# Kernel tuning notes

Measured on AMD Instinct MI355X. Metric: run time of the kernel, lower is better.

Reference implementation:

```python
import jax, jax.numpy as jnp
import numpy as np

B, L, H, E, R = 2, 512, 768, 512, 32768
H2 = H // 2


def setup_inputs() -> dict:
    key = jax.random.key(0)
    ks = jax.random.split(key, 16)
    s = 0.02
    inp = {
        "hidden_states": jax.random.normal(ks[0], (B, L, H), dtype=jnp.float32),
        "ent_start": jax.random.randint(ks[1], (B, E), 0, L, dtype=jnp.int32),
        "ent_label": jax.random.randint(ks[2], (B, E), 0, 3, dtype=jnp.int32),
        "rel_head": jax.random.randint(ks[3], (B, R), 0, E, dtype=jnp.int32),
        "rel_tail": jax.random.randint(ks[4], (B, R), 0, E, dtype=jnp.int32),
        "rel_label": jax.random.randint(ks[5], (B, R), 0, 2, dtype=jnp.int32),
        "entity_emb": jax.random.normal(ks[6], (3, H), dtype=jnp.float32) * s,
        "head_W1": jax.random.normal(ks[7], (2 * H, H), dtype=jnp.float32) * s,
        "head_b1": jnp.zeros((H,), dtype=jnp.float32),
        "head_W2": jax.random.normal(ks[8], (H, H2), dtype=jnp.float32) * s,
        "head_b2": jnp.zeros((H2,), dtype=jnp.float32),
        "tail_W1": jax.random.normal(ks[9], (2 * H, H), dtype=jnp.float32) * s,
        "tail_b1": jnp.zeros((H,), dtype=jnp.float32),
        "tail_W2": jax.random.normal(ks[10], (H, H2), dtype=jnp.float32) * s,
        "tail_b2": jnp.zeros((H2,), dtype=jnp.float32),
        "bil_W": jax.random.normal(ks[11], (2, H2, H2), dtype=jnp.float32) * s,
        "lin_W": jax.random.normal(ks[12], (2 * H2, 2), dtype=jnp.float32) * s,
        "lin_b": jnp.zeros((2,), dtype=jnp.float32),
    }
    return inp


def _mlp(x, W1, b1, W2, b2):
    # Linear -> ReLU -> (dropout=identity) -> Linear -> ReLU -> (dropout=identity)
    h = jax.nn.relu(jnp.einsum("brd,dh->brh", x, W1) + b1)
    return jax.nn.relu(jnp.einsum("brh,hk->brk", h, W2) + b2)


def reference(hidden_states, ent_start, ent_label, rel_head, rel_tail, rel_label,
              entity_emb, head_W1, head_b1, head_W2, head_b2,
              tail_W1, tail_b1, tail_W2, tail_b2, bil_W, lin_W, lin_b):
    # Gather entity start token index and label for each relation endpoint
    h_idx = jnp.take_along_axis(ent_start, rel_head, axis=1)  # [B,R]
    t_idx = jnp.take_along_axis(ent_start, rel_tail, axis=1)
    h_lab = jnp.take_along_axis(ent_label, rel_head, axis=1)
    t_lab = jnp.take_along_axis(ent_label, rel_tail, axis=1)

    # Gather hidden states at entity start positions: [B,R,H]
    h_tok = jnp.take_along_axis(hidden_states, h_idx[..., None], axis=1)
    t_tok = jnp.take_along_axis(hidden_states, t_idx[..., None], axis=1)

    head_repr = jnp.concatenate([h_tok, entity_emb[h_lab]], axis=-1)  # [B,R,2H]
    tail_repr = jnp.concatenate([t_tok, entity_emb[t_lab]], axis=-1)

    heads = _mlp(head_repr, head_W1, head_b1, head_W2, head_b2)  # [B,R,H2]
    tails = _mlp(tail_repr, tail_W1, tail_b1, tail_W2, tail_b2)

    # BiaffineAttention: bilinear(x1,x2) + linear(cat(x1,x2))
    bil = jnp.einsum("brd,ode,bre->bro", heads, bil_W, tails)  # [B,R,2]
    lin = jnp.einsum("brc,co->bro", jnp.concatenate([heads, tails], axis=-1), lin_W) + lin_b
    logits = bil + lin  # [B,R,2]

    # Per-doc mean cross-entropy, summed over docs (matches loss accumulation)
    logp = jax.nn.log_softmax(logits, axis=-1)
    ce = -jnp.take_along_axis(logp, rel_label[..., None], axis=-1)[..., 0]  # [B,R]
    loss = ce.mean(axis=-1).sum()

    return loss, logits.reshape(B * R, 2)
```

## Files before the change

### kernel.cpp

```cpp
#include <hip/hip_runtime.h>
#include <math.h>

#define BB 2
#define LL 512
#define HH 768
#define EE 512
#define RR 32768
#define H2 384
#define MM 1024

typedef __attribute__((ext_vector_type(8))) short     bf16x8;
typedef __attribute__((ext_vector_type(4))) float     f32x4;
typedef __attribute__((ext_vector_type(8))) unsigned short u16x8;

#define BUFE (64 * 72)

__device__ __forceinline__ unsigned short f2bf(float f) {
    unsigned int u = __float_as_uint(f);
    u = (u + 0x7FFFu + ((u >> 16) & 1u)) >> 16;
    return (unsigned short)u;
}

__device__ __forceinline__ void wtrans(const float* __restrict__ src,
                                       unsigned short* __restrict__ dst,
                                       int K, int N, int tile, unsigned short* T)
{
    const int t = threadIdx.x;
    const int tn = N >> 5;
    const int n0 = (tile % tn) * 32;
    const int k0 = (tile / tn) * 32;
    const int r  = t >> 3;
    const int c4 = (t & 7) * 4;
    const float4 g = *(const float4*)(src + (size_t)(k0 + r) * N + n0 + c4);
    T[(c4 + 0) * 40 + r] = f2bf(g.x);
    T[(c4 + 1) * 40 + r] = f2bf(g.y);
    T[(c4 + 2) * 40 + r] = f2bf(g.z);
    T[(c4 + 3) * 40 + r] = f2bf(g.w);
    __syncthreads();
    const int n  = t >> 3;
    const int k4 = (t & 7) * 4;
    *(ushort4*)(dst + (size_t)(n0 + n) * K + k0 + k4) = *(ushort4*)&T[n * 40 + k4];
}

__global__ __launch_bounds__(256) void prep(
    const float* __restrict__ hW1, const float* __restrict__ tW1,
    unsigned short* __restrict__ W1ht, unsigned short* __restrict__ W1tt,
    const float* __restrict__ hidden, const int* __restrict__ ent_start,
    const float* __restrict__ emb,
    const float* __restrict__ hb1, const float* __restrict__ tb1,
    unsigned short* __restrict__ Hbf, float* __restrict__ embc,
    float* __restrict__ hlin, float* __restrict__ tlin, float* __restrict__ out)
{
    __shared__ unsigned short T[32 * 40];
    __shared__ float red[4][192];
    const int bid = blockIdx.x;
    const int t = threadIdx.x;

    if (bid == 2200) {
        const float4 z = {0.f, 0.f, 0.f, 0.f};
        ((float4*)hlin)[t] = z; ((float4*)hlin)[256 + t] = z;
        ((float4*)tlin)[t] = z; ((float4*)tlin)[256 + t] = z;
        if (t == 0) out[0] = 0.f;
        return;
    }

    if (bid >= 2176) {
        const int eb = bid - 2176;
        const int tc = t & 63;
        const int kg = t >> 6;
        const int n = eb * 64 + tc;
        const float* W = (n < 768) ? hW1 : tW1;
        const int cc = (n < 768) ? n : n - 768;
        float a0 = 0.f, a1 = 0.f, a2 = 0.f;
        const int kbeg = kg * 192;
        #pragma unroll 8
        for (int k = kbeg; k < kbeg + 192; ++k) {
            const float w = W[(size_t)(768 + k) * 768 + cc];
            a0 += emb[k] * w;
            a1 += emb[768 + k] * w;
            a2 += emb[1536 + k] * w;
        }
        red[kg][0 * 64 + tc] = a0;
        red[kg][1 * 64 + tc] = a1;
        red[kg][2 * 64 + tc] = a2;
        __syncthreads();
        if (kg == 0) {
            const float b = (n < 768) ? hb1[n] : tb1[n - 768];
            #pragma unroll
            for (int l = 0; l < 3; ++l) {
                embc[l * 1536 + n] = b + red[0][l * 64 + tc] + red[1][l * 64 + tc]
                                       + red[2][l * 64 + tc] + red[3][l * 64 + tc];
            }
        }
        return;
    }

    if (bid >= 1152) {
        const int m = bid - 1152;
        if (t >= 96) return;
        const int b = m >> 9;
        const int idx = ent_start[m];
        const float4* s = (const float4*)(hidden + (size_t)(b * LL + idx) * HH);
        const float4 v0 = s[2 * t];
        const float4 v1 = s[2 * t + 1];
        u16x8 o;
        o[0] = f2bf(v0.x); o[1] = f2bf(v0.y); o[2] = f2bf(v0.z); o[3] = f2bf(v0.w);
        o[4] = f2bf(v1.x); o[5] = f2bf(v1.y); o[6] = f2bf(v1.z); o[7] = f2bf(v1.w);
        *(u16x8*)(Hbf + (size_t)m * 768 + 8 * t) = o;
        return;
    }

    if (bid < 576) wtrans(hW1, W1ht, 768, 768, bid, T);
    else           wtrans(tW1, W1tt, 768, 768, bid - 576, T);
}

template<bool RELU, bool BIAS, bool EB, bool WF32, bool WBF16, bool O2, bool LIN>
__device__ __forceinline__ void gemm_body(
    int tile, int nx,
    const unsigned short* __restrict__ A, int lda, int aoff1,
    const unsigned short* __restrict__ Bt0, const unsigned short* __restrict__ Bt1,
    int ldb, int bt_mrow, int Nh,
    const float* __restrict__ bias0, const float* __restrict__ bias1,
    const float* __restrict__ embc, const int* __restrict__ labels,
    const float* __restrict__ linW, float* __restrict__ hlin, float* __restrict__ tlin,
    int K, float* __restrict__ Cf, unsigned short* __restrict__ Cb, int ldc,
    unsigned short* As, unsigned short* Bs)
{
    const int tid = threadIdx.x;
    const int n0 = (tile % nx) * 64;
    const int m0 = (tile / nx) * 64;
    const int hf = (n0 >= Nh) ? 1 : 0;
    const unsigned short* Bt = hf ? Bt1 : Bt0;
    const int nc0 = n0 - (hf ? Nh : 0);
    const int aoff = hf ? aoff1 : 0;

    const int sr = tid >> 2;
    const int sk = (tid & 3) * 16;

    const unsigned short* Ap = A + (size_t)(m0 + sr) * lda + aoff + sk;
    const unsigned short* Bp = Bt + (size_t)((m0 >> 9) * bt_mrow + nc0 + sr) * ldb + sk;

    const int lane = tid & 63;
    const int wave = tid >> 6;
    const int wm = (wave & 1) * 32;
    const int wn = (wave >> 1) * 32;
    const int l15 = lane & 15;
    const int quad = lane >> 4;
    const int swo = sr * 72 + sk;
    const int aro = quad * 8;

    f32x4 acc00 = {}, acc01 = {}, acc10 = {}, acc11 = {};

    u16x8 pa0, pa1, pb0, pb1;
    u16x8 qa0, qa1, qb0, qb1;

#define GLOADP(ko) { pa0 = *(const u16x8*)(Ap + (ko)); pa1 = *(const u16x8*)(Ap + (ko) + 8); \
                     pb0 = *(const u16x8*)(Bp + (ko)); pb1 = *(const u16x8*)(Bp + (ko) + 8); }
#define GLOADQ(ko) { qa0 = *(const u16x8*)(Ap + (ko)); qa1 = *(const u16x8*)(Ap + (ko) + 8); \
                     qb0 = *(const u16x8*)(Bp + (ko)); qb1 = *(const u16x8*)(Bp + (ko) + 8); }
#define SWRITEP(bi) { unsigned short* Aw = As + (bi) * BUFE; unsigned short* Bw = Bs + (bi) * BUFE; \
                      *(u16x8*)&Aw[swo] = pa0; *(u16x8*)&Aw[swo + 8] = pa1; \
                      *(u16x8*)&Bw[swo] = pb0; *(u16x8*)&Bw[swo + 8] = pb1; }
#define SWRITEQ(bi) { unsigned short* Aw = As + (bi) * BUFE; unsigned short* Bw = Bs + (bi) * BUFE; \
                      *(u16x8*)&Aw[swo] = qa0; *(u16x8*)&Aw[swo + 8] = qa1; \
                      *(u16x8*)&Bw[swo] = qb0; *(u16x8*)&Bw[swo + 8] = qb1; }
#define BAR() { asm volatile("s_waitcnt lgkmcnt(0)" ::: "memory"); \
                __builtin_amdgcn_s_barrier(); \
                __builtin_amdgcn_sched_barrier(0); }
#define MFMA8(bi) { const unsigned short* Ac = As + (bi) * BUFE; \
                    const unsigned short* Bc = Bs + (bi) * BUFE; \
        const bf16x8 fa0 = *(const bf16x8*)&Ac[(wm + l15) * 72 + aro]; \
        const bf16x8 fa1 = *(const bf16x8*)&Ac[(wm + 16 + l15) * 72 + aro]; \
        const bf16x8 fb0 = *(const bf16x8*)&Bc[(wn + l15) * 72 + aro]; \
        const bf16x8 fb1 = *(const bf16x8*)&Bc[(wn + 16 + l15) * 72 + aro]; \
        const bf16x8 ga0 = *(const bf16x8*)&Ac[(wm + l15) * 72 + aro + 32]; \
        const bf16x8 ga1 = *(const bf16x8*)&Ac[(wm + 16 + l15) * 72 + aro + 32]; \
        const bf16x8 gb0 = *(const bf16x8*)&Bc[(wn + l15) * 72 + aro + 32]; \
        const bf16x8 gb1 = *(const bf16x8*)&Bc[(wn + 16 + l15) * 72 + aro + 32]; \
        acc00 = __builtin_amdgcn_mfma_f32_16x16x32_bf16(fa0, fb0, acc00, 0, 0, 0); \
        acc01 = __builtin_amdgcn_mfma_f32_16x16x32_bf16(fa0, fb1, acc01, 0, 0, 0); \
        acc10 = __builtin_amdgcn_mfma_f32_16x16x32_bf16(fa1, fb0, acc10, 0, 0, 0); \
        acc11 = __builtin_amdgcn_mfma_f32_16x16x32_bf16(fa1, fb1, acc11, 0, 0, 0); \
        acc00 = __builtin_amdgcn_mfma_f32_16x16x32_bf16(ga0, gb0, acc00, 0, 0, 0); \
        acc01 = __builtin_amdgcn_mfma_f32_16x16x32_bf16(ga0, gb1, acc01, 0, 0, 0); \
        acc10 = __builtin_amdgcn_mfma_f32_16x16x32_bf16(ga1, gb0, acc10, 0, 0, 0); \
        acc11 = __builtin_amdgcn_mfma_f32_16x16x32_bf16(ga1, gb1, acc11, 0, 0, 0); }

    const int NT = K >> 6;

    GLOADP(0);
    GLOADQ(64);
    SWRITEP(0);

    for (int it = 0; it < NT; it += 2) {
        BAR();
        if (it + 2 < NT) GLOADP((it + 2) << 6);
        MFMA8(0);
        SWRITEQ(1);
        BAR();
        if (it + 3 < NT) GLOADQ((it + 3) << 6);
        MFMA8(1);
        if (it + 2 < NT) SWRITEP(0);
    }

#undef GLOADP
#undef GLOADQ
#undef SWRITEP
#undef SWRITEQ
#undef BAR
#undef MFMA8

    float bias_v0 = 0.f, bias_v1 = 0.f;
    if (BIAS) {
        const float* bb = hf ? bias1 : bias0;
        bias_v0 = bb[nc0 + wn + l15];
        bias_v1 = bb[nc0 + wn + 16 + l15];
    }
    const int col0 = n0 + wn + l15;
    const int col1 = col0 + 16;
    int colw0 = col0, colw1 = col1;
    if (O2) {
        colw0 = 2 * (nc0 + wn + l15) + hf;
        colw1 = 2 * (nc0 + wn + 16 + l15) + hf;
    }
    float2 lw0 = {0.f, 0.f}, lw1 = {0.f, 0.f};
    float* lout = nullptr;
    if (LIN) {
        lw0 = ((const float2*)linW)[col0];
        lw1 = ((const float2*)linW)[col1];
        lout = hf ? tlin : hlin;
    }
    const f32x4 accs[2][2] = {{acc00, acc01}, {acc10, acc11}};
    #pragma unroll
    for (int mi = 0; mi < 2; ++mi) {
        #pragma unroll
        for (int r = 0; r < 4; ++r) {
            const int row = m0 + wm + mi * 16 + quad * 4 + r;
            float v0 = accs[mi][0][r];
            float v1 = accs[mi][1][r];
            if (BIAS) { v0 += bias_v0; v1 += bias_v1; }
            if (EB) {
                const int lab = labels[row];
                v0 += embc[lab * 1536 + col0];
                v1 += embc[lab * 1536 + col1];
            }
            if (RELU) { v0 = fmaxf(v0, 0.f); v1 = fmaxf(v1, 0.f); }
            if (WF32) {
                Cf[(size_t)row * ldc + colw0] = v0;
                Cf[(size_t)row * ldc + colw1] = v1;
            }
            if (WBF16) {
                Cb[(size_t)row * ldc + colw0] = f2bf(v0);
                Cb[(size_t)row * ldc + colw1] = f2bf(v1);
            }
            if (LIN) {
                float s0 = v0 * lw0.x + v1 * lw1.x;
                float s1 = v0 * lw0.y + v1 * lw1.y;
                #pragma unroll
                for (int o = 8; o >= 1; o >>= 1) {
                    s0 += __shfl_xor(s0, o, 64);
                    s1 += __shfl_xor(s1, o, 64);
                }
                if (l15 == 0) {
                    atomicAdd(&lout[2 * row],     s0);
                    atomicAdd(&lout[2 * row + 1], s1);
                }
            }
        }
    }
}

template<bool RELU, bool BIAS, bool EB, bool WF32, bool WBF16, bool O2, bool LIN>
__global__ __launch_bounds__(256) void gemm_mfma(
    const unsigned short* __restrict__ A, int lda, int aoff1,
    const unsigned short* __restrict__ Bt0, const unsigned short* __restrict__ Bt1,
    int ldb, int bt_mrow, int Nh,
    const float* __restrict__ bias0, const float* __restrict__ bias1,
    const float* __restrict__ embc, const int* __restrict__ labels,
    const float* __restrict__ linW, float* __restrict__ hlin, float* __restrict__ tlin,
    int K, float* __restrict__ Cf, unsigned short* __restrict__ Cb, int ldc)
{
    __shared__ __align__(16) unsigned short As[2 * BUFE];
    __shared__ __align__(16) unsigned short Bs[2 * BUFE];
    gemm_body<RELU, BIAS, EB, WF32, WBF16, O2, LIN>(
        blockIdx.y * gridDim.x + blockIdx.x, gridDim.x,
        A, lda, aoff1, Bt0, Bt1, ldb, bt_mrow, Nh,
        bias0, bias1, embc, labels, linW, hlin, tlin,
        K, Cf, Cb, ldc, As, Bs);
}

__global__ __launch_bounds__(256) void gemm1_plus(
    const unsigned short* __restrict__ Hbf,
    const unsigned short* __restrict__ W1ht, const unsigned short* __restrict__ W1tt,
    const float* __restrict__ embc, const int* __restrict__ ent_label,
    unsigned short* __restrict__ Y1bf,
    const float* __restrict__ hW2, const float* __restrict__ tW2,
    const float* __restrict__ bilW,
    unsigned short* __restrict__ W2ht, unsigned short* __restrict__ W2tt,
    unsigned short* __restrict__ bW0t, unsigned short* __restrict__ bW1t)
{
    __shared__ __align__(16) unsigned short As[2 * BUFE];
    __shared__ __align__(16) unsigned short Bs[2 * BUFE];
    const int bid = blockIdx.x;
    if (bid >= 384) {
        const int task = bid - 384;
        if (task < 288)      wtrans(hW2, W2ht, 768, 384, task, As);
        else if (task < 576) wtrans(tW2, W2tt, 768, 384, task - 288, As);
        else if (task < 720) wtrans(bilW, bW0t, 384, 384, task - 576, As);
        else                 wtrans(bilW + 384 * 384, bW1t, 384, 384, task - 720, As);
        return;
    }
    gemm_body<true, false, true, false, true, false, false>(
        bid, 24, Hbf, 768, 0, W1ht, W1tt, 768, 0, 768,
        nullptr, nullptr, embc, ent_label, nullptr, nullptr, nullptr,
        768, nullptr, Y1bf, 1536, As, Bs);
}

__global__ __launch_bounds__(256) void rel_gather(
    const float* __restrict__ Stab,
    const float* __restrict__ hlin, const float* __restrict__ tlin,
    const float* __restrict__ lin_b,
    const int* __restrict__ rel_head, const int* __restrict__ rel_tail,
    const int* __restrict__ rel_label,
    float* __restrict__ out)
{
    const int tid = threadIdx.x;
    const int i = blockIdx.x * 256 + tid;
    const int b = i >> 15;
    const int h = rel_head[i];
    const int t = rel_tail[i];
    const int lab = rel_label[i];
    const int mh = (b << 9) + h;
    const int mt = (b << 9) + t;

    const float2 hl = ((const float2*)hlin)[mh];
    const float2 tl = ((const float2*)tlin)[mt];
    const float2 zz = *(const float2*)(Stab + (size_t)mh * 1024 + 2 * t);
    const float z0 = zz.x + hl.x + tl.x + lin_b[0];
    const float z1 = zz.y + hl.y + tl.y + lin_b[1];
    out[1 + 2 * (size_t)i] = z0;
    out[2 + 2 * (size_t)i] = z1;

    const float mx = fmaxf(z0, z1);
    const float mn = fminf(z0, z1);
    const float lse = mx + log1pf(expf(mn - mx));
    float ce = lse - (lab ? z1 : z0);

    #pragma unroll
    for (int o = 32; o >= 1; o >>= 1) ce += __shfl_xor(ce, o, 64);
    __shared__ float wsum[4];
    if ((tid & 63) == 0) wsum[tid >> 6] = ce;
    __syncthreads();
    if (tid == 0) {
        const float bs = wsum[0] + wsum[1] + wsum[2] + wsum[3];
        atomicAdd(out, bs * (1.0f / (float)RR));
    }
}

extern "C" void kernel_launch(void* const* d_in, const int* in_sizes, int n_in,
                              void* d_out, int out_size, void* d_ws, size_t ws_size,
                              hipStream_t stream) {
    const float* hidden    = (const float*)d_in[0];
    const int*   ent_start = (const int*)d_in[1];
    const int*   ent_label = (const int*)d_in[2];
    const int*   rel_head  = (const int*)d_in[3];
    const int*   rel_tail  = (const int*)d_in[4];
    const int*   rel_label = (const int*)d_in[5];
    const float* emb       = (const float*)d_in[6];
    const float* head_W1   = (const float*)d_in[7];
    const float* head_b1   = (const float*)d_in[8];
    const float* head_W2   = (const float*)d_in[9];
    const float* head_b2   = (const float*)d_in[10];
    const float* tail_W1   = (const float*)d_in[11];
    const float* tail_b1   = (const float*)d_in[12];
    const float* tail_W2   = (const float*)d_in[13];
    const float* tail_b2   = (const float*)d_in[14];
    const float* bil_W     = (const float*)d_in[15];
    const float* lin_W     = (const float*)d_in[16];
    const float* lin_b     = (const float*)d_in[17];
    float* out = (float*)d_out;

    char* w = (char*)d_ws;
    auto carve = [&](size_t bytes) {
        char* p = w; w += (bytes + 255) & ~(size_t)255; return p;
    };
    unsigned short* Hbf  = (unsigned short*)carve((size_t)MM * 768 * 2);
    unsigned short* Y1bf = (unsigned short*)carve((size_t)MM * 1536 * 2);
    unsigned short* HTbf = (unsigned short*)carve((size_t)MM * 768 * 2);
    unsigned short* hWbf = (unsigned short*)carve((size_t)MM * 768 * 2);
    float*          Stab = (float*)carve((size_t)MM * 1024 * 4);
    unsigned short* W1ht = (unsigned short*)carve((size_t)768 * 768 * 2);
    unsigned short* W1tt = (unsigned short*)carve((size_t)768 * 768 * 2);
    unsigned short* W2ht = (unsigned short*)carve((size_t)384 * 768 * 2);
    unsigned short* W2tt = (unsigned short*)carve((size_t)384 * 768 * 2);
    unsigned short* bW0t = (unsigned short*)carve((size_t)384 * 384 * 2);
    unsigned short* bW1t = (unsigned short*)carve((size_t)384 * 384 * 2);
    float*          embc = (float*)carve((size_t)3 * 1536 * 4);
    float*          hlin = (float*)carve(2048 * 4);
    float*          tlin = (float*)carve(2048 * 4);

    prep<<<2201, 256, 0, stream>>>(
        head_W1, tail_W1, W1ht, W1tt,
        hidden, ent_start, emb, head_b1, tail_b1, Hbf, embc,
        hlin, tlin, out);

    gemm1_plus<<<1248, 256, 0, stream>>>(
        Hbf, W1ht, W1tt, embc, ent_label, Y1bf,
        head_W2, tail_W2, bil_W, W2ht, W2tt, bW0t, bW1t);

    gemm_mfma<true, true, false, false, true, false, true>
        <<<dim3(12, 16), 256, 0, stream>>>(
        Y1bf, 1536, 768, W2ht, W2tt, 768, 0, 384, head_b2, tail_b2,
        nullptr, nullptr, lin_W, hlin, tlin, 768, nullptr, HTbf, 768);

    gemm_mfma<false, false, false, false, true, false, false>
        <<<dim3(12, 16), 256, 0, stream>>>(
        HTbf, 768, 0, bW0t, bW1t, 384, 0, 384, nullptr, nullptr,
        nullptr, nullptr, nullptr, nullptr, nullptr, 384, nullptr, hWbf, 768);

    gemm_mfma<false, false, false, true, false, true, false>
        <<<dim3(16, 16), 256, 0, stream>>>(
        hWbf, 768, 384, HTbf + 384, HTbf + 384, 768, 512, 512,
        nullptr, nullptr, nullptr, nullptr, nullptr, nullptr, nullptr,
        384, Stab, nullptr, 1024);

    rel_gather<<<256, 256, 0, stream>>>(Stab, hlin, tlin, lin_b,
                                        rel_head, rel_tail, rel_label, out);
}
```

Before: 143.1 us.

## Fuse pairwise score GEMM with relation gather and loss into one kernel

Replaces the all-pairs bilinear score GEMM, which wrote a full fp32 score table to global memory, and the separate relation-gather kernel with one fused kernel. Each block computes a 64x32 tile of head-by-tail scores for both output channels into shared memory. It then scans all relations and handles those whose head and tail fall in its tile, writing logits and adding to the loss. This removes the 4 MB score-table round trip and one launch. The cost is that every one of the 256 blocks reads all 65536 relation indices, and the simpler single-buffer GEMM loop has less load/compute overlap.

```diff
diff --git a/kernel.cpp b/kernel.cpp
--- a/kernel.cpp
+++ b/kernel.cpp
@@ -114,16 +114,16 @@
     else           wtrans(tW1, W1tt, 768, 768, bid - 576, T);
 }
 
-template<bool RELU, bool BIAS, bool EB, bool WF32, bool WBF16, bool O2, bool LIN>
+template<bool RELU, bool BIAS, bool EB, bool WBF16, bool LIN>
 __device__ __forceinline__ void gemm_body(
     int tile, int nx,
     const unsigned short* __restrict__ A, int lda, int aoff1,
     const unsigned short* __restrict__ Bt0, const unsigned short* __restrict__ Bt1,
-    int ldb, int bt_mrow, int Nh,
+    int ldb, int Nh,
     const float* __restrict__ bias0, const float* __restrict__ bias1,
     const float* __restrict__ embc, const int* __restrict__ labels,
     const float* __restrict__ linW, float* __restrict__ hlin, float* __restrict__ tlin,
-    int K, float* __restrict__ Cf, unsigned short* __restrict__ Cb, int ldc,
+    int K, unsigned short* __restrict__ Cb, int ldc,
     unsigned short* As, unsigned short* Bs)
 {
     const int tid = threadIdx.x;
@@ -138,7 +138,7 @@
     const int sk = (tid & 3) * 16;
 
     const unsigned short* Ap = A + (size_t)(m0 + sr) * lda + aoff + sk;
-    const unsigned short* Bp = Bt + (size_t)((m0 >> 9) * bt_mrow + nc0 + sr) * ldb + sk;
+    const unsigned short* Bp = Bt + (size_t)(nc0 + sr) * ldb + sk;
 
     const int lane = tid & 63;
     const int wave = tid >> 6;
@@ -218,11 +218,6 @@
     }
     const int col0 = n0 + wn + l15;
     const int col1 = col0 + 16;
-    int colw0 = col0, colw1 = col1;
-    if (O2) {
-        colw0 = 2 * (nc0 + wn + l15) + hf;
-        colw1 = 2 * (nc0 + wn + 16 + l15) + hf;
-    }
     float2 lw0 = {0.f, 0.f}, lw1 = {0.f, 0.f};
     float* lout = nullptr;
     if (LIN) {
@@ -245,13 +240,9 @@
                 v1 += embc[lab * 1536 + col1];
             }
             if (RELU) { v0 = fmaxf(v0, 0.f); v1 = fmaxf(v1, 0.f); }
-            if (WF32) {
-                Cf[(size_t)row * ldc + colw0] = v0;
-                Cf[(size_t)row * ldc + colw1] = v1;
-            }
             if (WBF16) {
-                Cb[(size_t)row * ldc + colw0] = f2bf(v0);
-                Cb[(size_t)row * ldc + colw1] = f2bf(v1);
+                Cb[(size_t)row * ldc + col0] = f2bf(v0);
+                Cb[(size_t)row * ldc + col1] = f2bf(v1);
             }
             if (LIN) {
                 float s0 = v0 * lw0.x + v1 * lw1.x;
@@ -270,23 +261,23 @@
     }
 }
 
-template<bool RELU, bool BIAS, bool EB, bool WF32, bool WBF16, bool O2, bool LIN>
+template<bool RELU, bool BIAS, bool EB, bool WBF16, bool LIN>
 __global__ __launch_bounds__(256) void gemm_mfma(
     const unsigned short* __restrict__ A, int lda, int aoff1,
     const unsigned short* __restrict__ Bt0, const unsigned short* __restrict__ Bt1,
-    int ldb, int bt_mrow, int Nh,
+    int ldb, int Nh,
     const float* __restrict__ bias0, const float* __restrict__ bias1,
     const float* __restrict__ embc, const int* __restrict__ labels,
     const float* __restrict__ linW, float* __restrict__ hlin, float* __restrict__ tlin,
-    int K, float* __restrict__ Cf, unsigned short* __restrict__ Cb, int ldc)
+    int K, unsigned short* __restrict__ Cb, int ldc)
 {
     __shared__ __align__(16) unsigned short As[2 * BUFE];
     __shared__ __align__(16) unsigned short Bs[2 * BUFE];
-    gemm_body<RELU, BIAS, EB, WF32, WBF16, O2, LIN>(
+    gemm_body<RELU, BIAS, EB, WBF16, LIN>(
         blockIdx.y * gridDim.x + blockIdx.x, gridDim.x,
-        A, lda, aoff1, Bt0, Bt1, ldb, bt_mrow, Nh,
+        A, lda, aoff1, Bt0, Bt1, ldb, Nh,
         bias0, bias1, embc, labels, linW, hlin, tlin,
-        K, Cf, Cb, ldc, As, Bs);
+        K, Cb, ldc, As, Bs);
 }
 
 __global__ __launch_bounds__(256) void gemm1_plus(
@@ -310,51 +301,121 @@
         else                 wtrans(bilW + 384 * 384, bW1t, 384, 384, task - 720, As);
         return;
     }
-    gemm_body<true, false, true, false, true, false, false>(
-        bid, 24, Hbf, 768, 0, W1ht, W1tt, 768, 0, 768,
+    gemm_body<true, false, true, true, false>(
+        bid, 24, Hbf, 768, 0, W1ht, W1tt, 768, 768,
         nullptr, nullptr, embc, ent_label, nullptr, nullptr, nullptr,
-        768, nullptr, Y1bf, 1536, As, Bs);
-}
-
-__global__ __launch_bounds__(256) void rel_gather(
-    const float* __restrict__ Stab,
+        768, Y1bf, 1536, As, Bs);
+}
+
+__global__ __launch_bounds__(256) void score_rel(
+    const unsigned short* __restrict__ hWbf, const unsigned short* __restrict__ HTbf,
     const float* __restrict__ hlin, const float* __restrict__ tlin,
     const float* __restrict__ lin_b,
     const int* __restrict__ rel_head, const int* __restrict__ rel_tail,
     const int* __restrict__ rel_label,
     float* __restrict__ out)
 {
+    __shared__ __align__(16) unsigned short As[2][64 * 72];
+    __shared__ __align__(16) unsigned short Bs[2][32 * 72];
+    __shared__ float wsum[4];
+
     const int tid = threadIdx.x;
-    const int i = blockIdx.x * 256 + tid;
-    const int b = i >> 15;
-    const int h = rel_head[i];
-    const int t = rel_tail[i];
-    const int lab = rel_label[i];
-    const int mh = (b << 9) + h;
-    const int mt = (b << 9) + t;
-
-    const float2 hl = ((const float2*)hlin)[mh];
-    const float2 tl = ((const float2*)tlin)[mt];
-    const float2 zz = *(const float2*)(Stab + (size_t)mh * 1024 + 2 * t);
-    const float z0 = zz.x + hl.x + tl.x + lin_b[0];
-    const float z1 = zz.y + hl.y + tl.y + lin_b[1];
-    out[1 + 2 * (size_t)i] = z0;
-    out[2 + 2 * (size_t)i] = z1;
-
-    const float mx = fmaxf(z0, z1);
-    const float mn = fminf(z0, z1);
-    const float lse = mx + log1pf(expf(mn - mx));
-    float ce = lse - (lab ? z1 : z0);
-
+    const int t0 = blockIdx.x * 32;
+    const int m0 = blockIdx.y * 64;
+    const int batch = m0 >> 9;
+
+    const int asr = tid >> 2;
+    const int ask = (tid & 3) * 16;
+    const unsigned short* Ap = hWbf + (size_t)(m0 + asr) * 768 + ask;
+    const int bsr = tid >> 3;
+    const int bsk = (tid & 7) * 8;
+    const unsigned short* Bp = HTbf + (size_t)(batch * 512 + t0 + bsr) * 768 + 384 + bsk;
+
+    const int lane = tid & 63;
+    const int wave = tid >> 6;
+    const int wm = (wave & 1) * 32;
+    const int wn = (wave >> 1) * 16;
+    const int l15 = lane & 15;
+    const int quad = lane >> 4;
+    const int aro = quad * 8;
+
+    f32x4 p00 = {}, p01 = {};
+    f32x4 p10 = {}, p11 = {};
+
+    for (int it = 0; it < 12; ++it) {
+        const int koA = (it < 6) ? it * 64 : (it - 6) * 64 + 384;
+        const int koB = ((it < 6) ? it : it - 6) * 64;
+        const u16x8 av0 = *(const u16x8*)(Ap + koA);
+        const u16x8 av1 = *(const u16x8*)(Ap + koA + 8);
+        const u16x8 bv  = *(const u16x8*)(Bp + koB);
+        __syncthreads();
+        *(u16x8*)&As[it & 1][asr * 72 + ask]     = av0;
+        *(u16x8*)&As[it & 1][asr * 72 + ask + 8] = av1;
+        *(u16x8*)&Bs[it & 1][bsr * 72 + bsk]     = bv;
+        __syncthreads();
+        const unsigned short* Ac = As[it & 1];
+        const unsigned short* Bc = Bs[it & 1];
+        const bf16x8 fa0 = *(const bf16x8*)&Ac[(wm + l15) * 72 + aro];
+        const bf16x8 fa1 = *(const bf16x8*)&Ac[(wm + 16 + l15) * 72 + aro];
+        const bf16x8 fb  = *(const bf16x8*)&Bc[(wn + l15) * 72 + aro];
+        const bf16x8 ga0 = *(const bf16x8*)&Ac[(wm + l15) * 72 + aro + 32];
+        const bf16x8 ga1 = *(const bf16x8*)&Ac[(wm + 16 + l15) * 72 + aro + 32];
+        const bf16x8 gb  = *(const bf16x8*)&Bc[(wn + l15) * 72 + aro + 32];
+        if (it < 6) {
+            p00 = __builtin_amdgcn_mfma_f32_16x16x32_bf16(fa0, fb, p00, 0, 0, 0);
+            p01 = __builtin_amdgcn_mfma_f32_16x16x32_bf16(fa1, fb, p01, 0, 0, 0);
+            p00 = __builtin_amdgcn_mfma_f32_16x16x32_bf16(ga0, gb, p00, 0, 0, 0);
+            p01 = __builtin_amdgcn_mfma_f32_16x16x32_bf16(ga1, gb, p01, 0, 0, 0);
+        } else {
+            p10 = __builtin_amdgcn_mfma_f32_16x16x32_bf16(fa0, fb, p10, 0, 0, 0);
+            p11 = __builtin_amdgcn_mfma_f32_16x16x32_bf16(fa1, fb, p11, 0, 0, 0);
+            p10 = __builtin_amdgcn_mfma_f32_16x16x32_bf16(ga0, gb, p10, 0, 0, 0);
+            p11 = __builtin_amdgcn_mfma_f32_16x16x32_bf16(ga1, gb, p11, 0, 0, 0);
+        }
+    }
+
+    __syncthreads();
+    float* Sl = (float*)&As[0][0];
+    const int col = wn + l15;
+    #pragma unroll
+    for (int mi = 0; mi < 2; ++mi) {
+        #pragma unroll
+        for (int r = 0; r < 4; ++r) {
+            const int row = wm + mi * 16 + quad * 4 + r;
+            Sl[row * 33 + col]           = mi ? p01[r] : p00[r];
+            Sl[64 * 33 + row * 33 + col] = mi ? p11[r] : p10[r];
+        }
+    }
+    __syncthreads();
+
+    const float lb0 = lin_b[0], lb1 = lin_b[1];
+    float ce = 0.f;
+    for (int j = tid; j < BB * RR; j += 256) {
+        const int boff = (j >> 15) << 9;
+        const int mh = boff + rel_head[j];
+        if ((unsigned)(mh - m0) < 64u) {
+            const int t = rel_tail[j];
+            if ((unsigned)(t - t0) < 32u) {
+                const int mt = boff + t;
+                const float2 hl = ((const float2*)hlin)[mh];
+                const float2 tl = ((const float2*)tlin)[mt];
+                const int so = (mh - m0) * 33 + (t - t0);
+                const float z0 = Sl[so]           + hl.x + tl.x + lb0;
+                const float z1 = Sl[64 * 33 + so] + hl.y + tl.y + lb1;
+                out[1 + 2 * (size_t)j] = z0;
+                out[2 + 2 * (size_t)j] = z1;
+                const float mx = fmaxf(z0, z1);
+                const float mn = fminf(z0, z1);
+                ce += mx + log1pf(expf(mn - mx)) - (rel_label[j] ? z1 : z0);
+            }
+        }
+    }
     #pragma unroll
     for (int o = 32; o >= 1; o >>= 1) ce += __shfl_xor(ce, o, 64);
-    __shared__ float wsum[4];
-    if ((tid & 63) == 0) wsum[tid >> 6] = ce;
+    if (lane == 0) wsum[wave] = ce;
     __syncthreads();
-    if (tid == 0) {
-        const float bs = wsum[0] + wsum[1] + wsum[2] + wsum[3];
-        atomicAdd(out, bs * (1.0f / (float)RR));
-    }
+    if (tid == 0)
+        atomicAdd(out, (wsum[0] + wsum[1] + wsum[2] + wsum[3]) * (1.0f / (float)RR));
 }
 
 extern "C" void kernel_launch(void* const* d_in, const int* in_sizes, int n_in,
@@ -388,7 +449,6 @@
     unsigned short* Y1bf = (unsigned short*)carve((size_t)MM * 1536 * 2);
     unsigned short* HTbf = (unsigned short*)carve((size_t)MM * 768 * 2);
     unsigned short* hWbf = (unsigned short*)carve((size_t)MM * 768 * 2);
-    float*          Stab = (float*)carve((size_t)MM * 1024 * 4);
     unsigned short* W1ht = (unsigned short*)carve((size_t)768 * 768 * 2);
     unsigned short* W1tt = (unsigned short*)carve((size_t)768 * 768 * 2);
     unsigned short* W2ht = (unsigned short*)carve((size_t)384 * 768 * 2);
@@ -408,22 +468,17 @@
         Hbf, W1ht, W1tt, embc, ent_label, Y1bf,
         head_W2, tail_W2, bil_W, W2ht, W2tt, bW0t, bW1t);
 
-    gemm_mfma<true, true, false, false, true, false, true>
+    gemm_mfma<true, true, false, true, true>
         <<<dim3(12, 16), 256, 0, stream>>>(
-        Y1bf, 1536, 768, W2ht, W2tt, 768, 0, 384, head_b2, tail_b2,
-        nullptr, nullptr, lin_W, hlin, tlin, 768, nullptr, HTbf, 768);
-
-    gemm_mfma<false, false, false, false, true, false, false>
+        Y1bf, 1536, 768, W2ht, W2tt, 768, 384, head_b2, tail_b2,
+        nullptr, nullptr, lin_W, hlin, tlin, 768, HTbf, 768);
+
+    gemm_mfma<false, false, false, true, false>
         <<<dim3(12, 16), 256, 0, stream>>>(
-        HTbf, 768, 0, bW0t, bW1t, 384, 0, 384, nullptr, nullptr,
-        nullptr, nullptr, nullptr, nullptr, nullptr, 384, nullptr, hWbf, 768);
-
-    gemm_mfma<false, false, false, true, false, true, false>
-        <<<dim3(16, 16), 256, 0, stream>>>(
-        hWbf, 768, 384, HTbf + 384, HTbf + 384, 768, 512, 512,
-        nullptr, nullptr, nullptr, nullptr, nullptr, nullptr, nullptr,
-        384, Stab, nullptr, 1024);
-
-    rel_gather<<<256, 256, 0, stream>>>(Stab, hlin, tlin, lin_b,
-                                        rel_head, rel_tail, rel_label, out);
-}
+        HTbf, 768, 0, bW0t, bW1t, 384, 384, nullptr, nullptr,
+        nullptr, nullptr, nullptr, nullptr, nullptr, 384, hWbf, 768);
+
+    score_rel<<<dim3(16, 16), 256, 0, stream>>>(
+        hWbf, HTbf, hlin, tlin, lin_b,
+        rel_head, rel_tail, rel_label, out);
+}
```

Result: slower. 235.7 us (+64.8%).
